# Performance work log

Measured on AMD Instinct MI355X. Metric: run time of the kernel, lower is better.

The kernel has to match this reference:

```python
import jax, jax.numpy as jnp
import numpy as np

NUM_CODES = 1024
EMBED_DIM = 256
COMMITMENT_COST = 0.25


def setup_inputs() -> dict:
    key = jax.random.key(0)
    kz, kc = jax.random.split(key)
    z = jax.random.normal(kz, (131072, EMBED_DIM), dtype=jnp.float32)
    # codebook init matches nn.Embedding weight uniform_(-1/num_codes, 1/num_codes)
    codebook = jax.random.uniform(kc, (NUM_CODES, EMBED_DIM), dtype=jnp.float32,
                                  minval=-1.0 / NUM_CODES, maxval=1.0 / NUM_CODES)
    return {"z": z, "codebook": codebook}


def reference(z, codebook):
    # Squared-euclidean distances; argmin is identical to cdist (euclidean) argmin.
    z2 = jnp.sum(z * z, axis=-1, keepdims=True)            # [N, 1]
    c2 = jnp.sum(codebook * codebook, axis=-1)             # [K]
    d = z2 - 2.0 * (z @ codebook.T) + c2                   # [N, K]
    indices = jnp.argmin(d, axis=-1)                       # [N]
    zq = codebook[indices]                                 # [N, D] embedding lookup

    commitment_loss = COMMITMENT_COST * jnp.mean(
        (jax.lax.stop_gradient(zq) - z) ** 2)
    zq_st = z + jax.lax.stop_gradient(zq - z)              # straight-through
    residual = z - jax.lax.stop_gradient(zq)               # z - z_q.detach()

    counts = jnp.bincount(indices, length=NUM_CODES).astype(jnp.float32)
    avg_probs = counts / jnp.sum(counts)
    perplexity = jnp.exp(-jnp.sum(avg_probs * jnp.log(avg_probs + 1e-10)))

    return zq_st, residual, indices, commitment_loss, perplexity
```

## Files before the change

kernel.cpp:

```cpp
#include <hip/hip_runtime.h>
#include <math.h>

#define NR 131072
#define KC 1024
#define DD 256

#define ZQ_OFF  0
#define RES_OFF 33554432
#define IDX_OFF 67108864
#define LOSS_OFF 67239936
#define PERP_OFF 67239937

#define WS_CNT 0
#define WS_C2N 4096
#define WS_Z2  8192
#define WS_BSS 532480
#define WS_CBS 540672

#define MARG 5e-4f
#define CCAP 28

#define FM(x,y) __fmul_rn((x),(y))
#define FA(x,y) __fadd_rn((x),(y))

typedef __attribute__((ext_vector_type(8))) short bf16x8;
typedef __attribute__((ext_vector_type(4))) float f32x4;

static __device__ __forceinline__ unsigned short bf16h(float f) {
  unsigned int u = __float_as_uint(f);
  u += 0x7FFFu + ((u >> 16) & 1u);
  return (unsigned short)(u >> 16);
}

static __device__ __forceinline__ void glds16(const void* g, void* l) {
  __builtin_amdgcn_global_load_lds(
      (const __attribute__((address_space(1))) void*)g,
      (__attribute__((address_space(3))) void*)l, 16, 0, 0);
}

static __device__ __forceinline__ float np_sumsq128(const float* __restrict__ q) {
  float lane[16];
#pragma unroll
  for (int l = 0; l < 16; l++) {
    float s0 = FM(q[l +   0], q[l +   0]);
    float s1 = FM(q[l +  16], q[l +  16]);
    float s2 = FM(q[l +  32], q[l +  32]);
    float s3 = FM(q[l +  48], q[l +  48]);
    float s4 = FM(q[l +  64], q[l +  64]);
    float s5 = FM(q[l +  80], q[l +  80]);
    float s6 = FM(q[l +  96], q[l +  96]);
    float s7 = FM(q[l + 112], q[l + 112]);
    lane[l] = FA(FA(FA(s0, s1), FA(s2, s3)), FA(FA(s4, s5), FA(s6, s7)));
  }
#pragma unroll
  for (int h = 8; h >= 1; h >>= 1)
#pragma unroll
    for (int l = 0; l < 8; l++)
      if (l < h) lane[l] = FA(lane[l], lane[l + h]);
  return lane[0];
}

static __device__ __forceinline__ float np_sumsq256(const float* __restrict__ p) {
  return FA(np_sumsq128(p), np_sumsq128(p + 128));
}

__global__ void vqn_c2(const float* __restrict__ cb, float* __restrict__ c2n) {
  const int code = blockIdx.x * 256 + threadIdx.x;
  if (code < KC) c2n[code] = np_sumsq256(cb + (size_t)code * DD);
}

__global__ void vqn_z2(const float* __restrict__ z, float* __restrict__ z2g) {
  const int row = blockIdx.x * 16 + (threadIdx.x >> 4);
  const int l   = threadIdx.x & 15;
  const float* q = z + (size_t)row * DD;
  float blk[2];
#pragma unroll
  for (int b = 0; b < 2; b++) {
    const float* qq = q + b * 128;
    const float s0 = FM(qq[l +   0], qq[l +   0]);
    const float s1 = FM(qq[l +  16], qq[l +  16]);
    const float s2 = FM(qq[l +  32], qq[l +  32]);
    const float s3 = FM(qq[l +  48], qq[l +  48]);
    const float s4 = FM(qq[l +  64], qq[l +  64]);
    const float s5 = FM(qq[l +  80], qq[l +  80]);
    const float s6 = FM(qq[l +  96], qq[l +  96]);
    const float s7 = FM(qq[l + 112], qq[l + 112]);
    float v = FA(FA(FA(s0, s1), FA(s2, s3)), FA(FA(s4, s5), FA(s6, s7)));
#pragma unroll
    for (int h = 8; h >= 1; h >>= 1) v = FA(v, __shfl_down(v, h, 16));
    blk[b] = v;
  }
  if (l == 0) z2g[row] = FA(blk[0], blk[1]);
}

__global__ void vqn_cbsplit(const float* __restrict__ cb,
                            unsigned short* __restrict__ cbs) {
  const int g  = blockIdx.x * 256 + threadIdx.x;
  const int t  = g >> 9;
  const int gi = g & 511;
  const int kc = gi >> 6, q = (gi >> 4) & 3, c = gi & 15;
  const float* src = cb + (size_t)(t * 16 + c) * DD + kc * 32 + q * 8;
  unsigned int w[4];
#pragma unroll
  for (int p = 0; p < 4; p++)
    w[p] = (unsigned int)bf16h(src[p * 2]) |
           ((unsigned int)bf16h(src[p * 2 + 1]) << 16);
  *(uint4*)(cbs + (size_t)g * 8) = make_uint4(w[0], w[1], w[2], w[3]);
}

__global__ __launch_bounds__(256, 4) void vqn_main(
    const float* __restrict__ z, const float* __restrict__ cb,
    const unsigned short* __restrict__ cbs,
    const float* __restrict__ c2n, const float* __restrict__ z2g,
    float* __restrict__ out, int* __restrict__ counts,
    double* __restrict__ bss) {
  __shared__ __align__(16) unsigned short ct[2][4096];
  __shared__ unsigned short ccode[128][CCAP];
  __shared__ float cd[128][CCAP];
  __shared__ int ccnt[128];
  __shared__ float m1row[128];
  __shared__ int rowidx[128];
  __shared__ double wred[4];

  const int tid = threadIdx.x, wg = blockIdx.x;
  const int wv = tid >> 6, ln = tid & 63;
  const int rl = ln & 15;
  const int qk = ln >> 4;
  const int rowg0 = wg * 128 + wv * 32 + rl;
  const float z2v0 = z2g[rowg0];
  const float z2v1 = z2g[rowg0 + 16];

  bf16x8 zH0[8], zH1[8];
#pragma unroll
  for (int kc = 0; kc < 8; kc++) {
    const float4* p0 = (const float4*)(z + (size_t)rowg0 * DD + kc * 32 + qk * 8);
    const float4* p1 = (const float4*)(z + (size_t)(rowg0 + 16) * DD + kc * 32 + qk * 8);
    const float4 a0 = p0[0], b0 = p0[1];
    const float4 a1 = p1[0], b1 = p1[1];
    zH0[kc][0] = (short)bf16h(a0.x); zH0[kc][1] = (short)bf16h(a0.y);
    zH0[kc][2] = (short)bf16h(a0.z); zH0[kc][3] = (short)bf16h(a0.w);
    zH0[kc][4] = (short)bf16h(b0.x); zH0[kc][5] = (short)bf16h(b0.y);
    zH0[kc][6] = (short)bf16h(b0.z); zH0[kc][7] = (short)bf16h(b0.w);
    zH1[kc][0] = (short)bf16h(a1.x); zH1[kc][1] = (short)bf16h(a1.y);
    zH1[kc][2] = (short)bf16h(a1.z); zH1[kc][3] = (short)bf16h(a1.w);
    zH1[kc][4] = (short)bf16h(b1.x); zH1[kc][5] = (short)bf16h(b1.y);
    zH1[kc][6] = (short)bf16h(b1.z); zH1[kc][7] = (short)bf16h(b1.w);
  }
  if (tid < 128) ccnt[tid] = 0;

#define STG(T, B) do {                                                        \
    _Pragma("unroll")                                                         \
    for (int u_ = 0; u_ < 2; u_++) {                                          \
      glds16(cbs + (size_t)(T) * 4096 + (size_t)((wv * 2 + u_) * 64 + ln) * 8,\
             &ct[B][(wv * 2 + u_) * 512]);                                    \
    }                                                                         \
  } while (0)

  float m10 = INFINITY, m11 = INFINITY;
  STG(0, 0);
#pragma unroll 1
  for (int t = 0; t < 64; t++) {
    if (t < 63) {
      STG(t + 1, (t + 1) & 1);
      asm volatile("s_waitcnt vmcnt(2)" ::: "memory");
    } else {
      asm volatile("s_waitcnt vmcnt(0)" ::: "memory");
    }
    __builtin_amdgcn_sched_barrier(0);
    __builtin_amdgcn_s_barrier();

    const unsigned short* cbuf = ct[t & 1];
    f32x4 accA = {0.f, 0.f, 0.f, 0.f}, accB = accA;
#pragma unroll
    for (int kc = 0; kc < 8; kc++) {
      const bf16x8 aH = *(const bf16x8*)&cbuf[kc * 512 + ln * 8];
      accA = __builtin_amdgcn_mfma_f32_16x16x32_bf16(aH, zH0[kc], accA, 0, 0, 0);
      accB = __builtin_amdgcn_mfma_f32_16x16x32_bf16(aH, zH1[kc], accB, 0, 0, 0);
    }
    float dh0[4], dh1[4];
#pragma unroll
    for (int r = 0; r < 4; r++) {
      const float c2v = c2n[t * 16 + qk * 4 + r];
      dh0[r] = z2v0 - 2.f * accA[r] + c2v;
      dh1[r] = z2v1 - 2.f * accB[r] + c2v;
      m10 = fminf(m10, dh0[r]);
      m11 = fminf(m11, dh1[r]);
    }
    m10 = fminf(m10, __shfl_xor(m10, 16));
    m10 = fminf(m10, __shfl_xor(m10, 32));
    m11 = fminf(m11, __shfl_xor(m11, 16));
    m11 = fminf(m11, __shfl_xor(m11, 32));
    const int rw0 = wv * 32 + rl;
#pragma unroll
    for (int r = 0; r < 4; r++) {
      if (dh0[r] <= m10 + MARG) {
        const int s = atomicAdd(&ccnt[rw0], 1);
        if (s < CCAP) {
          ccode[rw0][s] = (unsigned short)(t * 16 + qk * 4 + r);
          cd[rw0][s] = dh0[r];
        }
      }
      if (dh1[r] <= m11 + MARG) {
        const int s = atomicAdd(&ccnt[rw0 + 16], 1);
        if (s < CCAP) {
          ccode[rw0 + 16][s] = (unsigned short)(t * 16 + qk * 4 + r);
          cd[rw0 + 16][s] = dh1[r];
        }
      }
    }
    __builtin_amdgcn_s_barrier();
  }
#undef STG

  if (qk == 0) { m1row[wv * 32 + rl] = m10; m1row[wv * 32 + rl + 16] = m11; }
  __syncthreads();

  if (tid < 128) {
    const int row = wg * 128 + tid;
    const float mf = m1row[tid] + MARG;
    const int nc = ccnt[tid];
    int best;
    if (nc > CCAP) {
      const float* zr = z + (size_t)row * DD;
      const float z2r = z2g[row];
      float db = INFINITY; best = 0;
      for (int c = 0; c < KC; c++) {
        const float* cr = cb + (size_t)c * DD;
        float dot = 0.f;
#pragma unroll 8
        for (int k = 0; k < DD; k++) dot = __fmaf_rn(zr[k], cr[k], dot);
        const float t1 = 2.0f * dot;
        const float d = FA(FA(z2r, -t1), c2n[c]);
        if (d < db) { db = d; best = c; }
      }
    } else {
      int kept = 0, kcode = 0;
      for (int s = 0; s < nc; s++)
        if (cd[tid][s] <= mf) { kept++; kcode = ccode[tid][s]; }
      if (kept == 1) best = kcode;
      else {
        const float* zr = z + (size_t)row * DD;
        const float z2r = z2g[row];
        float db = INFINITY; int bi = 0x7FFFFFFF;
        for (int s = 0; s < nc; s++) {
          if (cd[tid][s] > mf) continue;
          const int c = ccode[tid][s];
          const float* cr = cb + (size_t)c * DD;
          float dot = 0.f;
#pragma unroll 8
          for (int k = 0; k < DD; k++) dot = __fmaf_rn(zr[k], cr[k], dot);
          const float t1 = 2.0f * dot;
          const float d = FA(FA(z2r, -t1), c2n[c]);
          if (d < db || (d == db && c < bi)) { db = d; bi = c; }
        }
        best = bi;
      }
    }
    rowidx[tid] = best;
    atomicAdd(&counts[best], 1);
    out[IDX_OFF + row] = (float)best;
  }
  __syncthreads();

  float ss = 0.f;
#pragma unroll 1
  for (int g = 0; g < 2; g++) {
    const int rr  = g * 64 + (tid >> 2);
    const int seg = tid & 3;
    const int id  = rowidx[rr];
    const size_t zrow = (size_t)(wg * 128 + rr) * DD + seg * 64;
    const float4* zp = (const float4*)(z + zrow);
    const float4* qp = (const float4*)(cb + (size_t)id * DD + seg * 64);
#pragma unroll
    for (int u = 0; u < 16; u++) {
      const float4 r4 = zp[u];
      const float4 q4 = qp[u];
      float4 stv, rsv; float dq;
      stv.x = r4.x + (q4.x - r4.x); rsv.x = r4.x - q4.x; dq = q4.x - r4.x; ss = fmaf(dq, dq, ss);
      stv.y = r4.y + (q4.y - r4.y); rsv.y = r4.y - q4.y; dq = q4.y - r4.y; ss = fmaf(dq, dq, ss);
      stv.z = r4.z + (q4.z - r4.z); rsv.z = r4.z - q4.z; dq = q4.z - r4.z; ss = fmaf(dq, dq, ss);
      stv.w = r4.w + (q4.w - r4.w); rsv.w = r4.w - q4.w; dq = q4.w - r4.w; ss = fmaf(dq, dq, ss);
      *(float4*)(out + ZQ_OFF  + zrow + u * 4) = stv;
      *(float4*)(out + RES_OFF + zrow + u * 4) = rsv;
    }
  }
  double dss = (double)ss;
  for (int o = 32; o; o >>= 1) dss += __shfl_down(dss, o, 64);
  if (ln == 0) wred[wv] = dss;
  __syncthreads();
  if (tid == 0) bss[wg] = wred[0] + wred[1] + wred[2] + wred[3];
}

__global__ void vqn_final(const int* __restrict__ counts,
                          const double* __restrict__ bss,
                          float* __restrict__ out) {
  __shared__ double red[256];
  const int t = threadIdx.x;
  double s = 0.0;
  for (int i = t; i < 1024; i += 256) s += bss[i];
  red[t] = s; __syncthreads();
  for (int s2 = 128; s2 > 0; s2 >>= 1) { if (t < s2) red[t] += red[t + s2]; __syncthreads(); }
  const double ssq = red[0];
  __syncthreads();
  double h = 0.0;
  for (int c = t; c < 1024; c += 256) {
    double p = (double)counts[c] / 131072.0;
    h += p * log(p + 1e-10);
  }
  red[t] = h; __syncthreads();
  for (int s2 = 128; s2 > 0; s2 >>= 1) { if (t < s2) red[t] += red[t + s2]; __syncthreads(); }
  if (t == 0) {
    out[LOSS_OFF] = (float)(0.25 * ssq / 33554432.0);
    out[PERP_OFF] = (float)exp(-red[0]);
  }
}

extern "C" void kernel_launch(void* const* d_in, const int* in_sizes, int n_in,
                              void* d_out, int out_size, void* d_ws, size_t ws_size,
                              hipStream_t stream) {
  const float* z;
  const float* cb;
  if (in_sizes[0] == NR * DD) { z = (const float*)d_in[0]; cb = (const float*)d_in[1]; }
  else                        { cb = (const float*)d_in[0]; z = (const float*)d_in[1]; }

  float* out = (float*)d_out;
  char* ws = (char*)d_ws;
  int*            counts = (int*)(ws + WS_CNT);
  float*          c2n    = (float*)(ws + WS_C2N);
  float*          z2g    = (float*)(ws + WS_Z2);
  double*         bssp   = (double*)(ws + WS_BSS);
  unsigned short* cbs    = (unsigned short*)(ws + WS_CBS);

  hipMemsetAsync(counts, 0, 4096, stream);
  vqn_c2<<<4, 256, 0, stream>>>(cb, c2n);
  vqn_cbsplit<<<128, 256, 0, stream>>>(cb, cbs);
  vqn_z2<<<NR / 16, 256, 0, stream>>>(z, z2g);
  vqn_main<<<NR / 128, 256, 0, stream>>>(z, cb, cbs, c2n, z2g, out, counts, bssp);
  vqn_final<<<1, 256, 0, stream>>>(counts, bssp, out);
}
```

Before: 370.4 us.

## Fuse row-norm computation into main kernel and restructure epilogue stores

Removes the separate z2 kernel and computes each row's squared norm inside the main kernel while the first codebook tile prefetch is in flight, keeping the norms in shared memory instead of a global workspace. The epilogue is rewritten so each wave handles one whole row per iteration, with each lane owning one float4, which gives fully contiguous 1KB row accesses. This drops one launch and a full extra read of z (128MB) plus the z2 round trip through global memory. In exchange, z is read again at the start of the main kernel and a block-wide barrier is added before the distance loop.

```diff
diff --git a/kernel.cpp b/kernel.cpp
--- a/kernel.cpp
+++ b/kernel.cpp
@@ -13,9 +13,8 @@
 
 #define WS_CNT 0
 #define WS_C2N 4096
-#define WS_Z2  8192
-#define WS_BSS 532480
-#define WS_CBS 540672
+#define WS_BSS 8192
+#define WS_CBS 16384
 
 #define MARG 5e-4f
 #define CCAP 28
@@ -64,36 +63,12 @@
   return FA(np_sumsq128(p), np_sumsq128(p + 128));
 }
 
-__global__ void vqn_c2(const float* __restrict__ cb, float* __restrict__ c2n) {
+__global__ void vqo_c2(const float* __restrict__ cb, float* __restrict__ c2n) {
   const int code = blockIdx.x * 256 + threadIdx.x;
   if (code < KC) c2n[code] = np_sumsq256(cb + (size_t)code * DD);
 }
 
-__global__ void vqn_z2(const float* __restrict__ z, float* __restrict__ z2g) {
-  const int row = blockIdx.x * 16 + (threadIdx.x >> 4);
-  const int l   = threadIdx.x & 15;
-  const float* q = z + (size_t)row * DD;
-  float blk[2];
-#pragma unroll
-  for (int b = 0; b < 2; b++) {
-    const float* qq = q + b * 128;
-    const float s0 = FM(qq[l +   0], qq[l +   0]);
-    const float s1 = FM(qq[l +  16], qq[l +  16]);
-    const float s2 = FM(qq[l +  32], qq[l +  32]);
-    const float s3 = FM(qq[l +  48], qq[l +  48]);
-    const float s4 = FM(qq[l +  64], qq[l +  64]);
-    const float s5 = FM(qq[l +  80], qq[l +  80]);
-    const float s6 = FM(qq[l +  96], qq[l +  96]);
-    const float s7 = FM(qq[l + 112], qq[l + 112]);
-    float v = FA(FA(FA(s0, s1), FA(s2, s3)), FA(FA(s4, s5), FA(s6, s7)));
-#pragma unroll
-    for (int h = 8; h >= 1; h >>= 1) v = FA(v, __shfl_down(v, h, 16));
-    blk[b] = v;
-  }
-  if (l == 0) z2g[row] = FA(blk[0], blk[1]);
-}
-
-__global__ void vqn_cbsplit(const float* __restrict__ cb,
+__global__ void vqo_cbsplit(const float* __restrict__ cb,
                             unsigned short* __restrict__ cbs) {
   const int g  = blockIdx.x * 256 + threadIdx.x;
   const int t  = g >> 9;
@@ -108,10 +83,10 @@
   *(uint4*)(cbs + (size_t)g * 8) = make_uint4(w[0], w[1], w[2], w[3]);
 }
 
-__global__ __launch_bounds__(256, 4) void vqn_main(
+__global__ __launch_bounds__(256, 4) void vqo_main(
     const float* __restrict__ z, const float* __restrict__ cb,
     const unsigned short* __restrict__ cbs,
-    const float* __restrict__ c2n, const float* __restrict__ z2g,
+    const float* __restrict__ c2n,
     float* __restrict__ out, int* __restrict__ counts,
     double* __restrict__ bss) {
   __shared__ __align__(16) unsigned short ct[2][4096];
@@ -119,6 +94,7 @@
   __shared__ float cd[128][CCAP];
   __shared__ int ccnt[128];
   __shared__ float m1row[128];
+  __shared__ float z2s[128];
   __shared__ int rowidx[128];
   __shared__ double wred[4];
 
@@ -127,8 +103,16 @@
   const int rl = ln & 15;
   const int qk = ln >> 4;
   const int rowg0 = wg * 128 + wv * 32 + rl;
-  const float z2v0 = z2g[rowg0];
-  const float z2v1 = z2g[rowg0 + 16];
+
+#define STG(T, B) do {                                                        \
+    _Pragma("unroll")                                                         \
+    for (int u_ = 0; u_ < 2; u_++) {                                          \
+      glds16(cbs + (size_t)(T) * 4096 + (size_t)((wv * 2 + u_) * 64 + ln) * 8,\
+             &ct[B][(wv * 2 + u_) * 512]);                                    \
+    }                                                                         \
+  } while (0)
+
+  STG(0, 0);
 
   bf16x8 zH0[8], zH1[8];
 #pragma unroll
@@ -146,18 +130,40 @@
     zH1[kc][4] = (short)bf16h(b1.x); zH1[kc][5] = (short)bf16h(b1.y);
     zH1[kc][6] = (short)bf16h(b1.z); zH1[kc][7] = (short)bf16h(b1.w);
   }
+
+  {
+    const int gg = ln >> 4, l = ln & 15;
+#pragma unroll 1
+    for (int g4 = 0; g4 < 8; g4++) {
+      const int rlcl = wv * 32 + g4 * 4 + gg;
+      const float* q = z + (size_t)(wg * 128 + rlcl) * DD;
+      float blk[2];
+#pragma unroll
+      for (int b = 0; b < 2; b++) {
+        const float* qq = q + b * 128;
+        const float s0 = FM(qq[l +   0], qq[l +   0]);
+        const float s1 = FM(qq[l +  16], qq[l +  16]);
+        const float s2 = FM(qq[l +  32], qq[l +  32]);
+        const float s3 = FM(qq[l +  48], qq[l +  48]);
+        const float s4 = FM(qq[l +  64], qq[l +  64]);
+        const float s5 = FM(qq[l +  80], qq[l +  80]);
+        const float s6 = FM(qq[l +  96], qq[l +  96]);
+        const float s7 = FM(qq[l + 112], qq[l + 112]);
+        float v = FA(FA(FA(s0, s1), FA(s2, s3)), FA(FA(s4, s5), FA(s6, s7)));
+#pragma unroll
+        for (int h = 8; h >= 1; h >>= 1) v = FA(v, __shfl_down(v, h, 16));
+        blk[b] = v;
+      }
+      if (l == 0) z2s[rlcl] = FA(blk[0], blk[1]);
+    }
+  }
   if (tid < 128) ccnt[tid] = 0;
-
-#define STG(T, B) do {                                                        \
-    _Pragma("unroll")                                                         \
-    for (int u_ = 0; u_ < 2; u_++) {                                          \
-      glds16(cbs + (size_t)(T) * 4096 + (size_t)((wv * 2 + u_) * 64 + ln) * 8,\
-             &ct[B][(wv * 2 + u_) * 512]);                                    \
-    }                                                                         \
-  } while (0)
+  __syncthreads();
+
+  const float z2v0 = z2s[wv * 32 + rl];
+  const float z2v1 = z2s[wv * 32 + rl + 16];
 
   float m10 = INFINITY, m11 = INFINITY;
-  STG(0, 0);
 #pragma unroll 1
   for (int t = 0; t < 64; t++) {
     if (t < 63) {
@@ -222,7 +228,7 @@
     int best;
     if (nc > CCAP) {
       const float* zr = z + (size_t)row * DD;
-      const float z2r = z2g[row];
+      const float z2r = z2s[tid];
       float db = INFINITY; best = 0;
       for (int c = 0; c < KC; c++) {
         const float* cr = cb + (size_t)c * DD;
@@ -240,7 +246,7 @@
       if (kept == 1) best = kcode;
       else {
         const float* zr = z + (size_t)row * DD;
-        const float z2r = z2g[row];
+        const float z2r = z2s[tid];
         float db = INFINITY; int bi = 0x7FFFFFFF;
         for (int s = 0; s < nc; s++) {
           if (cd[tid][s] > mf) continue;
@@ -264,25 +270,19 @@
 
   float ss = 0.f;
 #pragma unroll 1
-  for (int g = 0; g < 2; g++) {
-    const int rr  = g * 64 + (tid >> 2);
-    const int seg = tid & 3;
-    const int id  = rowidx[rr];
-    const size_t zrow = (size_t)(wg * 128 + rr) * DD + seg * 64;
-    const float4* zp = (const float4*)(z + zrow);
-    const float4* qp = (const float4*)(cb + (size_t)id * DD + seg * 64);
-#pragma unroll
-    for (int u = 0; u < 16; u++) {
-      const float4 r4 = zp[u];
-      const float4 q4 = qp[u];
-      float4 stv, rsv; float dq;
-      stv.x = r4.x + (q4.x - r4.x); rsv.x = r4.x - q4.x; dq = q4.x - r4.x; ss = fmaf(dq, dq, ss);
-      stv.y = r4.y + (q4.y - r4.y); rsv.y = r4.y - q4.y; dq = q4.y - r4.y; ss = fmaf(dq, dq, ss);
-      stv.z = r4.z + (q4.z - r4.z); rsv.z = r4.z - q4.z; dq = q4.z - r4.z; ss = fmaf(dq, dq, ss);
-      stv.w = r4.w + (q4.w - r4.w); rsv.w = r4.w - q4.w; dq = q4.w - r4.w; ss = fmaf(dq, dq, ss);
-      *(float4*)(out + ZQ_OFF  + zrow + u * 4) = stv;
-      *(float4*)(out + RES_OFF + zrow + u * 4) = rsv;
-    }
+  for (int g = 0; g < 32; g++) {
+    const int rlcl = wv * 32 + g;
+    const int id   = rowidx[rlcl];
+    const size_t zrow = (size_t)(wg * 128 + rlcl) * DD;
+    const float4 r4 = ((const float4*)(z  + zrow))[ln];
+    const float4 q4 = ((const float4*)(cb + (size_t)id * DD))[ln];
+    float4 stv, rsv; float dq;
+    stv.x = r4.x + (q4.x - r4.x); rsv.x = r4.x - q4.x; dq = q4.x - r4.x; ss = fmaf(dq, dq, ss);
+    stv.y = r4.y + (q4.y - r4.y); rsv.y = r4.y - q4.y; dq = q4.y - r4.y; ss = fmaf(dq, dq, ss);
+    stv.z = r4.z + (q4.z - r4.z); rsv.z = r4.z - q4.z; dq = q4.z - r4.z; ss = fmaf(dq, dq, ss);
+    stv.w = r4.w + (q4.w - r4.w); rsv.w = r4.w - q4.w; dq = q4.w - r4.w; ss = fmaf(dq, dq, ss);
+    ((float4*)(out + ZQ_OFF  + zrow))[ln] = stv;
+    ((float4*)(out + RES_OFF + zrow))[ln] = rsv;
   }
   double dss = (double)ss;
   for (int o = 32; o; o >>= 1) dss += __shfl_down(dss, o, 64);
@@ -291,7 +291,7 @@
   if (tid == 0) bss[wg] = wred[0] + wred[1] + wred[2] + wred[3];
 }
 
-__global__ void vqn_final(const int* __restrict__ counts,
+__global__ void vqo_final(const int* __restrict__ counts,
                           const double* __restrict__ bss,
                           float* __restrict__ out) {
   __shared__ double red[256];
@@ -327,14 +327,12 @@
   char* ws = (char*)d_ws;
   int*            counts = (int*)(ws + WS_CNT);
   float*          c2n    = (float*)(ws + WS_C2N);
-  float*          z2g    = (float*)(ws + WS_Z2);
   double*         bssp   = (double*)(ws + WS_BSS);
   unsigned short* cbs    = (unsigned short*)(ws + WS_CBS);
 
   hipMemsetAsync(counts, 0, 4096, stream);
-  vqn_c2<<<4, 256, 0, stream>>>(cb, c2n);
-  vqn_cbsplit<<<128, 256, 0, stream>>>(cb, cbs);
-  vqn_z2<<<NR / 16, 256, 0, stream>>>(z, z2g);
-  vqn_main<<<NR / 128, 256, 0, stream>>>(z, cb, cbs, c2n, z2g, out, counts, bssp);
-  vqn_final<<<1, 256, 0, stream>>>(counts, bssp, out);
-}
+  vqo_c2<<<4, 256, 0, stream>>>(cb, c2n);
+  vqo_cbsplit<<<128, 256, 0, stream>>>(cb, cbs);
+  vqo_main<<<NR / 128, 256, 0, stream>>>(z, cb, cbs, c2n, out, counts, bssp);
+  vqo_final<<<1, 256, 0, stream>>>(counts, bssp, out);
+}
```

Result: faster. 316.0 us (-14.7%).
